# Optimization experiments

Hardware: AMD Instinct MI355X
Metric: run time of the kernel (lower is better)

Reference implementation:

```python
import jax, jax.numpy as jnp
import numpy as np

TEMPERATURE = 0.5
EPS = 1e-8  # torch CosineSimilarity eps


def setup_inputs() -> dict:
    key = jax.random.key(0)
    # x holds 2*batch_size concatenated embeddings (two augmented views)
    x = jax.random.normal(key, (4096, 512), dtype=jnp.float32)
    return {"x": x}


def reference(x) -> jnp.ndarray:
    n2 = x.shape[0]          # 2N rows
    n = n2 // 2
    # cosine similarity: normalize rows (clamped norm as in torch), then GEMM
    norms = jnp.maximum(jnp.linalg.norm(x, axis=1, keepdims=True), EPS)
    xn = x / norms
    sim = jnp.einsum('id,jd->ij', xn, xn) / TEMPERATURE  # [2N, 2N]
    # positive logit for row i is sim[i, (i+N) mod 2N]
    idx = jnp.arange(n2)
    pos = sim[idx, (idx + n) % n2]
    # CE with label 0 over logits = [pos, negatives]; since the logit set for
    # row i is exactly {sim[i, j] : j != i}, CE_i = logsumexp_{j!=i} sim[i,j] - pos_i
    sim_masked = jnp.where(jnp.eye(n2, dtype=bool), -jnp.inf, sim)
    lse = jax.nn.logsumexp(sim_masked, axis=1)
    # criterion uses reduction='sum' then divides by bsz -> mean
    return jnp.mean(lse - pos)
```

## Files before the change

### kernel.cpp

```cpp
#include <hip/hip_runtime.h>
#include <hip/hip_bf16.h>
#include <math.h>

typedef __bf16 bf16_t;
typedef __bf16 bf16x8 __attribute__((ext_vector_type(8)));
typedef float f32x4 __attribute__((ext_vector_type(4)));

#define N2 4096
#define NHALF 2048
#define DIM 512
#define TEMP_INV 2.0f

__global__ __launch_bounds__(256) void k_normalize(const float* __restrict__ x,
                                                   bf16_t* __restrict__ xn) {
    const int row  = (blockIdx.x * blockDim.x + threadIdx.x) >> 6;
    const int lane = threadIdx.x & 63;
    const float4* xr = reinterpret_cast<const float4*>(x + (size_t)row * DIM);
    float4 a = xr[lane * 2];
    float4 b = xr[lane * 2 + 1];
    float ss = a.x*a.x + a.y*a.y + a.z*a.z + a.w*a.w
             + b.x*b.x + b.y*b.y + b.z*b.z + b.w*b.w;
#pragma unroll
    for (int off = 32; off; off >>= 1) ss += __shfl_xor(ss, off, 64);
    const float scale = 1.0f / fmaxf(sqrtf(ss), 1e-8f);
    float v[8] = {a.x, a.y, a.z, a.w, b.x, b.y, b.z, b.w};
    bf16x8 o;
#pragma unroll
    for (int t = 0; t < 8; ++t) o[t] = (bf16_t)(v[t] * scale);
    *reinterpret_cast<bf16x8*>(xn + (size_t)row * DIM + lane * 8) = o;
}

__global__ __launch_bounds__(256) void k_posdiag(const bf16_t* __restrict__ xn,
                                                 float* __restrict__ pos,
                                                 float* __restrict__ diag) {
    const int row  = (blockIdx.x * blockDim.x + threadIdx.x) >> 6;
    const int lane = threadIdx.x & 63;
    const int prow = (row + NHALF) & (N2 - 1);
    bf16x8 vi = *reinterpret_cast<const bf16x8*>(xn + (size_t)row  * DIM + lane * 8);
    bf16x8 vj = *reinterpret_cast<const bf16x8*>(xn + (size_t)prow * DIM + lane * 8);
    float dii = 0.0f, dij = 0.0f;
#pragma unroll
    for (int t = 0; t < 8; ++t) {
        float fi = (float)vi[t], fj = (float)vj[t];
        dii += fi * fi;
        dij += fi * fj;
    }
#pragma unroll
    for (int off = 32; off; off >>= 1) {
        dii += __shfl_xor(dii, off, 64);
        dij += __shfl_xor(dij, off, 64);
    }
    if (lane == 0) {
        pos[row]  = TEMP_INV * dij;
        diag[row] = TEMP_INV * dii;
    }
}

__device__ __forceinline__ void load_lds16(const bf16_t* g, bf16_t* l) {
    __builtin_amdgcn_global_load_lds(
        (const __attribute__((address_space(1))) unsigned int*)g,
        (__attribute__((address_space(3))) unsigned int*)l,
        16, 0, 0);
}

__global__ __launch_bounds__(256) void k_simgemm(const bf16_t* __restrict__ xn,
                                                 float* __restrict__ rowsum) {
    __shared__ bf16_t As[128 * 32];
    __shared__ bf16_t Bs[128 * 32];
    __shared__ float  rpart[128];

    const int tid  = threadIdx.x;
    const int lane = tid & 63;
    const int wid  = tid >> 6;
    const int wr   = wid >> 1;
    const int wc   = wid & 1;
    const int q    = lane >> 4;
    const int l15  = lane & 15;
    const int bm   = blockIdx.x;
    const int bn   = blockIdx.y;

    if (tid < 128) rpart[tid] = 0.0f;

    const int sRow = tid >> 2;
    const int sCol = (tid & 3) * 8;
    const bf16_t* gA0 = xn + (size_t)(bm * 128 + sRow) * DIM + sCol;
    const bf16_t* gB0 = xn + (size_t)(bn * 128 + sRow) * DIM + sCol;
    bf16_t* lA0 = &As[tid * 8];
    bf16_t* lA1 = &As[2048 + tid * 8];
    bf16_t* lB0 = &Bs[tid * 8];
    bf16_t* lB1 = &Bs[2048 + tid * 8];

    f32x4 acc[4][4] = {};

    for (int k0 = 0; k0 < DIM; k0 += 32) {
        __syncthreads();
        load_lds16(gA0 + k0, lA0);
        load_lds16(gA0 + (size_t)64 * DIM + k0, lA1);
        load_lds16(gB0 + k0, lB0);
        load_lds16(gB0 + (size_t)64 * DIM + k0, lB1);
        __syncthreads();

        bf16x8 af[4], bf[4];
#pragma unroll
        for (int mt = 0; mt < 4; ++mt)
            af[mt] = *reinterpret_cast<const bf16x8*>(
                &As[(wr * 64 + mt * 16 + l15) * 32 + q * 8]);
#pragma unroll
        for (int nt = 0; nt < 4; ++nt)
            bf[nt] = *reinterpret_cast<const bf16x8*>(
                &Bs[(wc * 64 + nt * 16 + l15) * 32 + q * 8]);
#pragma unroll
        for (int mt = 0; mt < 4; ++mt)
#pragma unroll
            for (int nt = 0; nt < 4; ++nt)
                acc[mt][nt] = __builtin_amdgcn_mfma_f32_16x16x32_bf16(
                    af[mt], bf[nt], acc[mt][nt], 0, 0, 0);
    }

#pragma unroll
    for (int mt = 0; mt < 4; ++mt) {
#pragma unroll
        for (int r = 0; r < 4; ++r) {
            float p = 0.0f;
#pragma unroll
            for (int nt = 0; nt < 4; ++nt)
                p += __expf(TEMP_INV * acc[mt][nt][r]);
            p += __shfl_xor(p, 1, 64);
            p += __shfl_xor(p, 2, 64);
            p += __shfl_xor(p, 4, 64);
            p += __shfl_xor(p, 8, 64);
            if (l15 == 0)
                atomicAdd(&rpart[wr * 64 + mt * 16 + q * 4 + r], p);
        }
    }
    __syncthreads();
    if (tid < 128) atomicAdd(&rowsum[bm * 128 + tid], rpart[tid]);
}

__global__ __launch_bounds__(256) void k_finalize(const float* __restrict__ rowsum,
                                                  const float* __restrict__ pos,
                                                  const float* __restrict__ diag,
                                                  float* __restrict__ out) {
    __shared__ float red[256];
    float s = 0.0f;
    for (int i = threadIdx.x; i < N2; i += 256)
        s += __logf(rowsum[i] - __expf(diag[i])) - pos[i];
    red[threadIdx.x] = s;
    __syncthreads();
    for (int st = 128; st; st >>= 1) {
        if (threadIdx.x < st) red[threadIdx.x] += red[threadIdx.x + st];
        __syncthreads();
    }
    if (threadIdx.x == 0) out[0] = red[0] / (float)N2;
}

extern "C" void kernel_launch(void* const* d_in, const int* in_sizes, int n_in,
                              void* d_out, int out_size, void* d_ws, size_t ws_size,
                              hipStream_t stream) {
    (void)in_sizes; (void)n_in; (void)out_size; (void)ws_size;
    const float* x = (const float*)d_in[0];
    float* out = (float*)d_out;

    char* ws = (char*)d_ws;
    bf16_t* xn     = (bf16_t*)ws;
    float*  rowsum = (float*)(ws + (size_t)N2 * DIM * 2);
    float*  pos    = rowsum + N2;
    float*  diag   = pos + N2;

    hipMemsetAsync(rowsum, 0, N2 * sizeof(float), stream);
    k_normalize<<<N2 / 4, 256, 0, stream>>>(x, xn);
    k_posdiag<<<N2 / 4, 256, 0, stream>>>(xn, pos, diag);
    dim3 grid(32, 32);
    k_simgemm<<<grid, 256, 0, stream>>>(xn, rowsum);
    k_finalize<<<1, 256, 0, stream>>>(rowsum, pos, diag, out);
}
```

Before: 98.10 us.

## Exploit similarity symmetry with triangular tile grid and fuse prep kernels

The GEMM now launches only the upper-triangular set of 128x128 tiles (528 instead of 1024) and uses the symmetry of the similarity matrix: each off-diagonal tile adds its exp values to both the row sums and the column sums. Normalization, positive and diagonal logit computation and zeroing of rowsum are fused into one prep kernel that handles row pairs i and i+N, which removes a launch, the memset and a reread of the normalized data. The cost is extra column reductions and shuffles, global atomics for two row ranges per tile, and a positive logit now taken from the fp32 dot product instead of bf16.

```diff
diff --git a/kernel.cpp b/kernel.cpp
--- a/kernel.cpp
+++ b/kernel.cpp
@@ -11,49 +11,64 @@
 #define DIM 512
 #define TEMP_INV 2.0f
 
-__global__ __launch_bounds__(256) void k_normalize(const float* __restrict__ x,
-                                                   bf16_t* __restrict__ xn) {
-    const int row  = (blockIdx.x * blockDim.x + threadIdx.x) >> 6;
+__global__ __launch_bounds__(256) void k_prep(const float* __restrict__ x,
+                                              bf16_t* __restrict__ xn,
+                                              float* __restrict__ pos,
+                                              float* __restrict__ diag,
+                                              float* __restrict__ rowsum) {
+    const int pair = blockIdx.x * 4 + (threadIdx.x >> 6);
     const int lane = threadIdx.x & 63;
-    const float4* xr = reinterpret_cast<const float4*>(x + (size_t)row * DIM);
-    float4 a = xr[lane * 2];
-    float4 b = xr[lane * 2 + 1];
-    float ss = a.x*a.x + a.y*a.y + a.z*a.z + a.w*a.w
-             + b.x*b.x + b.y*b.y + b.z*b.z + b.w*b.w;
-#pragma unroll
-    for (int off = 32; off; off >>= 1) ss += __shfl_xor(ss, off, 64);
-    const float scale = 1.0f / fmaxf(sqrtf(ss), 1e-8f);
-    float v[8] = {a.x, a.y, a.z, a.w, b.x, b.y, b.z, b.w};
-    bf16x8 o;
-#pragma unroll
-    for (int t = 0; t < 8; ++t) o[t] = (bf16_t)(v[t] * scale);
-    *reinterpret_cast<bf16x8*>(xn + (size_t)row * DIM + lane * 8) = o;
-}
-
-__global__ __launch_bounds__(256) void k_posdiag(const bf16_t* __restrict__ xn,
-                                                 float* __restrict__ pos,
-                                                 float* __restrict__ diag) {
-    const int row  = (blockIdx.x * blockDim.x + threadIdx.x) >> 6;
-    const int lane = threadIdx.x & 63;
-    const int prow = (row + NHALF) & (N2 - 1);
-    bf16x8 vi = *reinterpret_cast<const bf16x8*>(xn + (size_t)row  * DIM + lane * 8);
-    bf16x8 vj = *reinterpret_cast<const bf16x8*>(xn + (size_t)prow * DIM + lane * 8);
-    float dii = 0.0f, dij = 0.0f;
+    const int rowi = pair;
+    const int rowp = pair + NHALF;
+
+    const float4* xi = reinterpret_cast<const float4*>(x + (size_t)rowi * DIM);
+    const float4* xp = reinterpret_cast<const float4*>(x + (size_t)rowp * DIM);
+    float4 a0 = xi[lane * 2], a1 = xi[lane * 2 + 1];
+    float4 b0 = xp[lane * 2], b1 = xp[lane * 2 + 1];
+
+    float ssi = a0.x*a0.x + a0.y*a0.y + a0.z*a0.z + a0.w*a0.w
+              + a1.x*a1.x + a1.y*a1.y + a1.z*a1.z + a1.w*a1.w;
+    float ssp = b0.x*b0.x + b0.y*b0.y + b0.z*b0.z + b0.w*b0.w
+              + b1.x*b1.x + b1.y*b1.y + b1.z*b1.z + b1.w*b1.w;
+    float dot = a0.x*b0.x + a0.y*b0.y + a0.z*b0.z + a0.w*b0.w
+              + a1.x*b1.x + a1.y*b1.y + a1.z*b1.z + a1.w*b1.w;
+#pragma unroll
+    for (int off = 32; off; off >>= 1) {
+        ssi += __shfl_xor(ssi, off, 64);
+        ssp += __shfl_xor(ssp, off, 64);
+        dot += __shfl_xor(dot, off, 64);
+    }
+    const float ni = fmaxf(sqrtf(ssi), 1e-8f);
+    const float np = fmaxf(sqrtf(ssp), 1e-8f);
+    const float sci = 1.0f / ni, scp = 1.0f / np;
+
+    float va[8] = {a0.x, a0.y, a0.z, a0.w, a1.x, a1.y, a1.z, a1.w};
+    float vb[8] = {b0.x, b0.y, b0.z, b0.w, b1.x, b1.y, b1.z, b1.w};
+    bf16x8 oi, op;
+    float dii = 0.0f, dpp = 0.0f;
 #pragma unroll
     for (int t = 0; t < 8; ++t) {
-        float fi = (float)vi[t], fj = (float)vj[t];
+        oi[t] = (bf16_t)(va[t] * sci);
+        op[t] = (bf16_t)(vb[t] * scp);
+        float fi = (float)oi[t], fp_ = (float)op[t];
         dii += fi * fi;
-        dij += fi * fj;
-    }
+        dpp += fp_ * fp_;
+    }
+    *reinterpret_cast<bf16x8*>(xn + (size_t)rowi * DIM + lane * 8) = oi;
+    *reinterpret_cast<bf16x8*>(xn + (size_t)rowp * DIM + lane * 8) = op;
 #pragma unroll
     for (int off = 32; off; off >>= 1) {
         dii += __shfl_xor(dii, off, 64);
-        dij += __shfl_xor(dij, off, 64);
+        dpp += __shfl_xor(dpp, off, 64);
     }
     if (lane == 0) {
-        pos[row]  = TEMP_INV * dij;
-        diag[row] = TEMP_INV * dii;
-    }
+        const float pv = TEMP_INV * dot * sci * scp;
+        pos[rowi] = pv;
+        pos[rowp] = pv;
+        diag[rowi] = TEMP_INV * dii;
+        diag[rowp] = TEMP_INV * dpp;
+    }
+    if (threadIdx.x < 8) rowsum[blockIdx.x * 8 + threadIdx.x] = 0.0f;
 }
 
 __device__ __forceinline__ void load_lds16(const bf16_t* g, bf16_t* l) {
@@ -67,7 +82,15 @@
                                                  float* __restrict__ rowsum) {
     __shared__ bf16_t As[128 * 32];
     __shared__ bf16_t Bs[128 * 32];
-    __shared__ float  rpart[128];
+    __shared__ float  rpA[128];
+    __shared__ float  rpB[128];
+
+    const int t = blockIdx.x;
+    int bn = (int)((sqrtf(8.0f * (float)t + 1.0f) - 1.0f) * 0.5f);
+    while ((bn * (bn + 1)) / 2 > t) --bn;
+    while (((bn + 1) * (bn + 2)) / 2 <= t) ++bn;
+    const int bm = t - (bn * (bn + 1)) / 2;
+    const bool diagb = (bm == bn);
 
     const int tid  = threadIdx.x;
     const int lane = tid & 63;
@@ -76,10 +99,8 @@
     const int wc   = wid & 1;
     const int q    = lane >> 4;
     const int l15  = lane & 15;
-    const int bm   = blockIdx.x;
-    const int bn   = blockIdx.y;
-
-    if (tid < 128) rpart[tid] = 0.0f;
+
+    if (tid < 128) { rpA[tid] = 0.0f; rpB[tid] = 0.0f; }
 
     const int sRow = tid >> 2;
     const int sCol = (tid & 3) * 8;
@@ -117,24 +138,43 @@
                     af[mt], bf[nt], acc[mt][nt], 0, 0, 0);
     }
 
+    float colacc[4] = {0.0f, 0.0f, 0.0f, 0.0f};
 #pragma unroll
     for (int mt = 0; mt < 4; ++mt) {
+        float rowp[4] = {0.0f, 0.0f, 0.0f, 0.0f};
+#pragma unroll
+        for (int nt = 0; nt < 4; ++nt)
+#pragma unroll
+            for (int r = 0; r < 4; ++r) {
+                float e = __expf(TEMP_INV * acc[mt][nt][r]);
+                rowp[r] += e;
+                colacc[nt] += e;
+            }
 #pragma unroll
         for (int r = 0; r < 4; ++r) {
-            float p = 0.0f;
-#pragma unroll
-            for (int nt = 0; nt < 4; ++nt)
-                p += __expf(TEMP_INV * acc[mt][nt][r]);
+            float p = rowp[r];
             p += __shfl_xor(p, 1, 64);
             p += __shfl_xor(p, 2, 64);
             p += __shfl_xor(p, 4, 64);
             p += __shfl_xor(p, 8, 64);
-            if (l15 == 0)
-                atomicAdd(&rpart[wr * 64 + mt * 16 + q * 4 + r], p);
+            if (l15 == 0) atomicAdd(&rpA[wr * 64 + mt * 16 + q * 4 + r], p);
         }
     }
+    if (!diagb) {
+#pragma unroll
+        for (int nt = 0; nt < 4; ++nt) {
+            float c = colacc[nt];
+            c += __shfl_xor(c, 16, 64);
+            c += __shfl_xor(c, 32, 64);
+            if (q == 0) atomicAdd(&rpB[wc * 64 + nt * 16 + l15], c);
+        }
+    }
     __syncthreads();
-    if (tid < 128) atomicAdd(&rowsum[bm * 128 + tid], rpart[tid]);
+    if (tid < 128) {
+        atomicAdd(&rowsum[bm * 128 + tid], rpA[tid]);
+    } else if (!diagb) {
+        atomicAdd(&rowsum[bn * 128 + (tid - 128)], rpB[tid - 128]);
+    }
 }
 
 __global__ __launch_bounds__(256) void k_finalize(const float* __restrict__ rowsum,
@@ -167,10 +207,7 @@
     float*  pos    = rowsum + N2;
     float*  diag   = pos + N2;
 
-    hipMemsetAsync(rowsum, 0, N2 * sizeof(float), stream);
-    k_normalize<<<N2 / 4, 256, 0, stream>>>(x, xn);
-    k_posdiag<<<N2 / 4, 256, 0, stream>>>(xn, pos, diag);
-    dim3 grid(32, 32);
-    k_simgemm<<<grid, 256, 0, stream>>>(xn, rowsum);
+    k_prep<<<512, 256, 0, stream>>>(x, xn, pos, diag, rowsum);
+    k_simgemm<<<528, 256, 0, stream>>>(xn, rowsum);
     k_finalize<<<1, 256, 0, stream>>>(rowsum, pos, diag, out);
 }
```

Measured after the change: 82.42 us. 1.19x faster.
